# Kernel optimization log

Hardware: AMD Instinct MI355X
Metric: run time of the kernel (lower is better)

The kernel has to match this reference:

```python
import jax, jax.numpy as jnp
import numpy as np

B, T, D, H = 4, 2048, 1024, 8
HD = D // H  # head_dim = 128


def setup_inputs() -> dict:
    key = jax.random.key(0)
    ks = jax.random.split(key, 10)
    s = 1.0 / np.sqrt(D)
    return {
        "x": jax.random.normal(ks[0], (B, T, D), jnp.float32),
        "y": jax.random.normal(ks[1], (B, T, D), jnp.float32),
        "Wq": jax.random.normal(ks[2], (D, D), jnp.float32) * s,
        "bq": jnp.zeros((D,), jnp.float32),
        "Wk": jax.random.normal(ks[3], (D, D), jnp.float32) * s,
        "bk": jnp.zeros((D,), jnp.float32),
        "Wv": jax.random.normal(ks[4], (D, D), jnp.float32) * s,
        "bv": jnp.zeros((D,), jnp.float32),
        "Wo": jax.random.normal(ks[5], (D, D), jnp.float32) * s,
        "bo": jnp.zeros((D,), jnp.float32),
    }


def _heads(t):
    # [B, T, D] -> [B, H, T, HD]
    b, t_, _ = t.shape
    return t.reshape(b, t_, H, HD).transpose(0, 2, 1, 3)


def reference(x, y, Wq, bq, Wk, bk, Wv, bv, Wo, bo):
    Tq, Tk = x.shape[1], y.shape[1]
    q = _heads(x @ Wq.T + bq)  # [B,H,Tq,HD]
    k = _heads(y @ Wk.T + bk)  # [B,H,Tk,HD]
    v = _heads(y @ Wv.T + bv)  # [B,H,Tk,HD]
    scale = 1.0 / np.sqrt(HD)
    logits = jnp.einsum("bhqd,bhkd->bhqk", q, k) * scale
    # causal mask: positions k > q get -inf
    causal = jnp.triu(jnp.full((Tq, Tk), -jnp.inf, jnp.float32), k=1)
    logits = logits + causal
    attn = jax.nn.softmax(logits, axis=-1)  # [B,H,Tq,Tk]
    ctx = jnp.einsum("bhqk,bhkd->bhqd", attn, v)
    ctx = ctx.transpose(0, 2, 1, 3).reshape(x.shape[0], Tq, D)
    out = ctx @ Wo.T + bo
    return out
```

## Files before the change

### kernel.cpp

```cpp
#include <hip/hip_runtime.h>
#include <math.h>

#define TB 4
#define TT 2048
#define TD 1024
#define TH 8
#define THD 128

typedef __attribute__((ext_vector_type(8))) short short8;
typedef __attribute__((ext_vector_type(4))) short short4v;
typedef __attribute__((ext_vector_type(4))) float float4v;
typedef __attribute__((ext_vector_type(16))) float float16v;

__device__ __forceinline__ short f2bf(float f) {
    union { float f; unsigned u; } v; v.f = f;
    unsigned r = v.u + 0x7FFFu + ((v.u >> 16) & 1u);
    return (short)(r >> 16);
}

__device__ __forceinline__ float bf2f(short s) {
    union { unsigned u; float f; } v;
    v.u = ((unsigned)(unsigned short)s) << 16;
    return v.f;
}

__device__ __forceinline__ short8 cvt8(float4v a, float4v b) {
    short8 r;
    r[0] = f2bf(a[0]); r[1] = f2bf(a[1]); r[2] = f2bf(a[2]); r[3] = f2bf(a[3]);
    r[4] = f2bf(b[0]); r[5] = f2bf(b[1]); r[6] = f2bf(b[2]); r[7] = f2bf(b[3]);
    return r;
}

__device__ __forceinline__ void async16(const void* g, void* l) {
    __builtin_amdgcn_global_load_lds(
        (const __attribute__((address_space(1))) unsigned int*)g,
        (__attribute__((address_space(3))) unsigned int*)l, 16, 0, 0);
}

__global__ void cvtall(const float* __restrict__ x, const float* __restrict__ y,
                       const float* __restrict__ wq, const float* __restrict__ wk,
                       const float* __restrict__ wv, const float* __restrict__ wo,
                       short* __restrict__ xyb, short* __restrict__ wb)
{
    const size_t SZ = (size_t)TB * TT * TD;
    const size_t WSZ = (size_t)TD * TD;
    int ty = blockIdx.y;
    const float* s; short* d; size_t n;
    if (ty == 0)      { s = x;  d = xyb;      n = SZ; }
    else if (ty == 1) { s = y;  d = xyb + SZ; n = SZ; }
    else {
        s = (ty == 2) ? wq : (ty == 3) ? wk : (ty == 4) ? wv : wo;
        d = wb + (size_t)(ty - 2) * WSZ; n = WSZ;
    }
    size_t i = ((size_t)blockIdx.x * blockDim.x + threadIdx.x) * 8;
    if (i >= n) return;
    float4v v0 = *(const float4v*)(s + i);
    float4v v1 = *(const float4v*)(s + i + 4);
    *(short8*)(d + i) = cvt8(v0, v1);
}

__global__ __launch_bounds__(256, 2)
void gemm_qkv(const short* __restrict__ xyb, const short* __restrict__ wb,
              const float* __restrict__ bq, const float* __restrict__ bk,
              const float* __restrict__ bv,
              short* __restrict__ qhp, short* __restrict__ khp,
              short* __restrict__ vtp)
{
    __shared__ __attribute__((aligned(16))) short SMEM[16896];
    short* As = SMEM;
    short* Bs = SMEM + 8192;

    const int n0g = blockIdx.x * 128;
    const int mode = n0g >> 10;
    const int n0 = n0g & 1023;
    const int h_ = n0 >> 7;
    const size_t SZ = (size_t)TB * TT * TD;
    const short* A = (mode == 0) ? xyb : (xyb + SZ);
    const short* W = wb + (size_t)mode * TD * TD;
    const float* bias = (mode == 0) ? bq : (mode == 1) ? bk : bv;
    const float scale = (mode == 0)
        ? (0.08838834764831845f * 1.4426950408889634f) : 1.0f;

    const int tid = threadIdx.x;
    const int lane = tid & 63, wv = tid >> 6;
    const int lr = lane & 15, qd = lane >> 4;
    const int sw = lane & 7;
    const int wm = (wv >> 1) * 64, wn = (wv & 1) * 64;
    const int m0 = blockIdx.y * 128;
    const int K = TD;
    const int rsub = lane >> 3;
    const int gj = ((lane & 7) ^ rsub) * 8;

    float4v acc[4][4];
#pragma unroll
    for (int mt = 0; mt < 4; ++mt)
#pragma unroll
        for (int nt = 0; nt < 4; ++nt)
            acc[mt][nt] = float4v{0.f, 0.f, 0.f, 0.f};

    for (int kb = 0; kb < K; kb += 64) {
#pragma unroll
        for (int p = 0; p < 8; ++p) {
            int ch = wv * 8 + p;
            if (ch < 16) {
                int row = ch * 8 + rsub;
                async16(A + (size_t)(m0 + row) * K + kb + gj, As + ch * 512);
            } else {
                int row = (ch - 16) * 8 + rsub;
                async16(W + (size_t)(n0 + row) * K + kb + gj, Bs + (ch - 16) * 512);
            }
        }
        __syncthreads();

#pragma unroll
        for (int ks = 0; ks < 2; ++ks) {
            short8 af[4], bfr[4];
#pragma unroll
            for (int mt = 0; mt < 4; ++mt)
                af[mt] = *(const short8*)&As[(wm + mt * 16 + lr) * 64 +
                                             ((ks * 4 + qd) ^ sw) * 8];
#pragma unroll
            for (int nt = 0; nt < 4; ++nt)
                bfr[nt] = *(const short8*)&Bs[(wn + nt * 16 + lr) * 64 +
                                              ((ks * 4 + qd) ^ sw) * 8];
#pragma unroll
            for (int mt = 0; mt < 4; ++mt)
#pragma unroll
                for (int nt = 0; nt < 4; ++nt)
                    acc[mt][nt] = __builtin_amdgcn_mfma_f32_16x16x32_bf16(
                        af[mt], bfr[nt], acc[mt][nt], 0, 0, 0);
        }
        __syncthreads();
    }

#pragma unroll
    for (int nt = 0; nt < 4; ++nt) {
        int col = wn + nt * 16 + lr;
        float bi = bias[n0 + col];
#pragma unroll
        for (int mt = 0; mt < 4; ++mt)
#pragma unroll
            for (int i = 0; i < 4; ++i) {
                int row = wm + mt * 16 + qd * 4 + i;
                short v = f2bf((acc[mt][nt][i] + bi) * scale);
                if (mode < 2) SMEM[row * 128 + col] = v;
                else          SMEM[col * 132 + row] = v;
            }
    }
    __syncthreads();

    if (mode < 2) {
        short* outp = (mode == 0) ? qhp : khp;
#pragma unroll
        for (int r8 = 0; r8 < 8; ++r8) {
            int row = r8 * 16 + (tid >> 4), c = tid & 15;
            short8 v = *(const short8*)&SMEM[row * 128 + c * 8];
            int tg = m0 + row;
            int b_ = tg >> 11, t_ = tg & (TT - 1);
            *(short8*)&outp[(((size_t)(b_ * TH + h_)) * TT + t_) * THD + c * 8] = v;
        }
    } else {
        int b_ = m0 >> 11, t0 = m0 & (TT - 1);
#pragma unroll
        for (int r8 = 0; r8 < 8; ++r8) {
            int hd = r8 * 16 + (tid >> 4), c = tid & 15;
            short8 v = *(const short8*)&SMEM[hd * 132 + c * 8];
            *(short8*)&vtp[(((size_t)(b_ * TH + h_)) * THD + hd) * TT + t0 + c * 8] = v;
        }
    }
}

__global__ __launch_bounds__(256, 2)
void gemm_out(const short* __restrict__ A, const short* __restrict__ W,
              const float* __restrict__ bias, float* __restrict__ outp)
{
    __shared__ __attribute__((aligned(16))) short As[128 * 64];
    __shared__ __attribute__((aligned(16))) short Bs[128 * 64];

    const int tid = threadIdx.x;
    const int lane = tid & 63, wv = tid >> 6;
    const int lr = lane & 15, qd = lane >> 4;
    const int sw = lane & 7;
    const int wm = (wv >> 1) * 64, wn = (wv & 1) * 64;
    const int m0 = blockIdx.y * 128, n0 = blockIdx.x * 128;
    const int K = TD;
    const int rsub = lane >> 3;
    const int gj = ((lane & 7) ^ rsub) * 8;

    float4v acc[4][4];
#pragma unroll
    for (int mt = 0; mt < 4; ++mt)
#pragma unroll
        for (int nt = 0; nt < 4; ++nt)
            acc[mt][nt] = float4v{0.f, 0.f, 0.f, 0.f};

    for (int kb = 0; kb < K; kb += 64) {
#pragma unroll
        for (int p = 0; p < 8; ++p) {
            int ch = wv * 8 + p;
            if (ch < 16) {
                int row = ch * 8 + rsub;
                async16(A + (size_t)(m0 + row) * K + kb + gj, As + ch * 512);
            } else {
                int row = (ch - 16) * 8 + rsub;
                async16(W + (size_t)(n0 + row) * K + kb + gj, Bs + (ch - 16) * 512);
            }
        }
        __syncthreads();

#pragma unroll
        for (int ks = 0; ks < 2; ++ks) {
            short8 af[4], bfr[4];
#pragma unroll
            for (int mt = 0; mt < 4; ++mt)
                af[mt] = *(const short8*)&As[(wm + mt * 16 + lr) * 64 +
                                             ((ks * 4 + qd) ^ sw) * 8];
#pragma unroll
            for (int nt = 0; nt < 4; ++nt)
                bfr[nt] = *(const short8*)&Bs[(wn + nt * 16 + lr) * 64 +
                                              ((ks * 4 + qd) ^ sw) * 8];
#pragma unroll
            for (int mt = 0; mt < 4; ++mt)
#pragma unroll
                for (int nt = 0; nt < 4; ++nt)
                    acc[mt][nt] = __builtin_amdgcn_mfma_f32_16x16x32_bf16(
                        af[mt], bfr[nt], acc[mt][nt], 0, 0, 0);
        }
        __syncthreads();
    }

#pragma unroll
    for (int nt = 0; nt < 4; ++nt) {
        int col = n0 + wn + nt * 16 + lr;
        float bi = bias[col];
#pragma unroll
        for (int mt = 0; mt < 4; ++mt)
#pragma unroll
            for (int i = 0; i < 4; ++i) {
                int row = m0 + wm + mt * 16 + qd * 4 + i;
                outp[(size_t)row * TD + col] = acc[mt][nt][i] + bi;
            }
    }
}

__global__ __launch_bounds__(256, 2)
void attn_fwd(const short* __restrict__ qh, const short* __restrict__ kh,
              const short* __restrict__ vt, short* __restrict__ po,
              float* __restrict__ pl)
{
    __shared__ __attribute__((aligned(16))) short Ks[2][64 * 128];
    __shared__ __attribute__((aligned(16))) short Vs[2][128 * 64];

    const int tid = threadIdx.x;
    const int lane = tid & 63, wid = tid >> 6;
    const int l31 = lane & 31, h = lane >> 5;
    const int sw7 = l31 & 7;

    const int bi = blockIdx.x;
    const int bh = bi & 31;
    const int j  = bi >> 5;
    const size_t bho = (size_t)bh * TT * THD;

    for (int u = 0; u < 2; ++u) {
        const int qt  = u ? (15 - j) : j;
        const int kv0 = u ? (qt + 1) : 0;
        const int kv1 = u ? (2 * qt + 2) : (j + 1);

        short8 qf[8];
        {
            const short* qp = qh + bho + (size_t)(qt * 128 + wid * 32 + l31) * THD;
#pragma unroll
            for (int ks = 0; ks < 8; ++ks)
                qf[ks] = *(const short8*)(qp + ks * 16 + h * 8);
        }
        float16v o[4];
#pragma unroll
        for (int db = 0; db < 4; ++db)
#pragma unroll
            for (int r = 0; r < 16; ++r) o[db][r] = 0.f;
        float li = 0.f;

        {
            const short* kbase = kh + bho + (size_t)kv0 * 64 * THD;
            const short* vbase = vt + (size_t)bh * THD * TT + (size_t)kv0 * 64;
#pragma unroll
            for (int p = 0; p < 4; ++p) {
                int ch = wid * 4 + p;
                int kr = ch * 4 + (lane >> 4);
                int kg = (lane & 15) ^ (kr & 7);
                async16(kbase + (size_t)kr * THD + kg * 8, &Ks[0][ch * 512]);
                int vr = ch * 8 + (lane >> 3);
                int vg = (lane & 7) ^ (vr & 7);
                async16(vbase + (size_t)vr * TT + vg * 8, &Vs[0][ch * 512]);
            }
        }
        __syncthreads();

        int cur = 0;
        for (int kv = kv0; kv < kv1; ++kv) {
            if (kv + 1 < kv1) {
                const short* kbase = kh + bho + (size_t)(kv + 1) * 64 * THD;
                const short* vbase = vt + (size_t)bh * THD * TT +
                                     (size_t)(kv + 1) * 64;
#pragma unroll
                for (int p = 0; p < 4; ++p) {
                    int ch = wid * 4 + p;
                    int kr = ch * 4 + (lane >> 4);
                    int kg = (lane & 15) ^ (kr & 7);
                    async16(kbase + (size_t)kr * THD + kg * 8,
                            &Ks[cur ^ 1][ch * 512]);
                    int vr = ch * 8 + (lane >> 3);
                    int vg = (lane & 7) ^ (vr & 7);
                    async16(vbase + (size_t)vr * TT + vg * 8,
                            &Vs[cur ^ 1][ch * 512]);
                }
            }

            const short* Kc = Ks[cur];
            const short* Vc = Vs[cur];

            float16v s[2];
#pragma unroll
            for (int kb = 0; kb < 2; ++kb)
#pragma unroll
                for (int r = 0; r < 16; ++r) s[kb][r] = 0.f;
#pragma unroll
            for (int ks = 0; ks < 8; ++ks) {
                int cidx = ((ks * 2 + h) ^ sw7) * 8;
                short8 kf0 = *(const short8*)&Kc[l31 * 128 + cidx];
                short8 kf1 = *(const short8*)&Kc[(32 + l31) * 128 + cidx];
                s[0] = __builtin_amdgcn_mfma_f32_32x32x16_bf16(kf0, qf[ks], s[0], 0, 0, 0);
                s[1] = __builtin_amdgcn_mfma_f32_32x32x16_bf16(kf1, qf[ks], s[1], 0, 0, 0);
            }

            if (kv >= 2 * qt) {
                int q = qt * 128 + wid * 32 + l31;
#pragma unroll
                for (int r = 0; r < 16; ++r) {
                    int key = kv * 64 + (r & 3) + 8 * (r >> 2) + 4 * h;
                    if (key > q) s[0][r] = -1e30f;
                    if (key + 32 > q) s[1][r] = -1e30f;
                }
            }

#pragma unroll
            for (int st = 0; st < 8; ++st) {
                float e0 = exp2f(s[st >> 2][(st & 3) * 4 + 0]);
                float e1 = exp2f(s[st >> 2][(st & 3) * 4 + 1]);
                float e2 = exp2f(s[st >> 2][(st & 3) * 4 + 2]);
                float e3 = exp2f(s[st >> 2][(st & 3) * 4 + 3]);
                li += (e0 + e1) + (e2 + e3);
                short4v ap;
                ap[0] = f2bf(e0); ap[1] = f2bf(e1);
                ap[2] = f2bf(e2); ap[3] = f2bf(e3);
#pragma unroll
                for (int db = 0; db < 4; ++db) {
                    short4v vf = *(const short4v*)&Vc[(db * 32 + l31) * 64 +
                                                      ((st ^ sw7) * 8) + h * 4];
                    o[db] = __builtin_amdgcn_mfma_f32_32x32x8bf16_1k(ap, vf, o[db], 0, 0, 0);
                }
            }
            __syncthreads();
            cur ^= 1;
        }

        li += __shfl_xor(li, 32);
        const int slot = (bh * 16 + qt) * 2 + u;
        if (h == 0) pl[slot * 128 + wid * 32 + l31] = li;
        short* pop = po + (size_t)slot * 16384 + (size_t)(wid * 32) * 128 + l31;
#pragma unroll
        for (int r = 0; r < 16; ++r) {
            int ql = (r & 3) + 8 * (r >> 2) + 4 * h;
#pragma unroll
            for (int db = 0; db < 4; ++db)
                pop[(size_t)ql * 128 + db * 32] = f2bf(o[db][r]);
        }
    }
}

__global__ __launch_bounds__(256)
void combine(const short* __restrict__ po, const float* __restrict__ pl,
             short* __restrict__ ctx)
{
    const unsigned i = blockIdx.x * 256 + threadIdx.x;
    const int hdv = i & 15;
    const int q   = (i >> 4) & 127;
    const int qt  = (i >> 11) & 15;
    const int bh  = i >> 15;
    const int tile = bh * 16 + qt;
    const size_t base = (size_t)tile * 2 * 16384 + (size_t)q * 128 + hdv * 8;
    short8 a = *(const short8*)&po[base];
    short8 b = *(const short8*)&po[base + 16384];
    const float inv = 1.f / (pl[tile * 2 * 128 + q] + pl[(tile * 2 + 1) * 128 + q]);
    short8 r;
#pragma unroll
    for (int k = 0; k < 8; ++k)
        r[k] = f2bf((bf2f(a[k]) + bf2f(b[k])) * inv);
    const int b_ = bh >> 3, h_ = bh & 7, t = qt * 128 + q;
    *(short8*)&ctx[((size_t)(b_ * TT + t)) * TD + h_ * THD + hdv * 8] = r;
}

extern "C" void kernel_launch(void* const* d_in, const int* in_sizes, int n_in,
                              void* d_out, int out_size, void* d_ws, size_t ws_size,
                              hipStream_t stream) {
    (void)in_sizes; (void)n_in; (void)out_size; (void)ws_size;
    const float* x  = (const float*)d_in[0];
    const float* y  = (const float*)d_in[1];
    const float* Wq = (const float*)d_in[2];
    const float* bq = (const float*)d_in[3];
    const float* Wk = (const float*)d_in[4];
    const float* bk = (const float*)d_in[5];
    const float* Wv = (const float*)d_in[6];
    const float* bv = (const float*)d_in[7];
    const float* Wo = (const float*)d_in[8];
    const float* bo = (const float*)d_in[9];
    float* out = (float*)d_out;

    const size_t SZ = (size_t)TB * TT * TD;
    const size_t WSZ = (size_t)TD * TD;
    short* xyb = (short*)d_ws;
    short* wb  = xyb + 2 * SZ;
    short* qh  = wb + 4 * WSZ;
    short* kh  = qh + SZ;
    short* vt  = kh + SZ;
    float* pl  = (float*)(vt + SZ);
    short* po  = xyb;
    short* ctx = qh;

    dim3 blk(256);

    hipLaunchKernelGGL(cvtall, dim3(SZ / 2048, 6), blk, 0, stream,
                       x, y, Wq, Wk, Wv, Wo, xyb, wb);
    hipLaunchKernelGGL(gemm_qkv, dim3(24, 64), blk, 0, stream,
                       xyb, wb, bq, bk, bv, qh, kh, vt);
    hipLaunchKernelGGL(attn_fwd, dim3(512), blk, 0, stream, qh, kh, vt, po, pl);
    hipLaunchKernelGGL(combine, dim3(4096), blk, 0, stream, po, pl, ctx);
    hipLaunchKernelGGL(gemm_out, dim3(8, 64), blk, 0, stream,
                       ctx, wb + 3 * WSZ, bo, out);
}
```

Baseline: 292.9 us.

## Rewrite projection GEMMs as 256x128 double-buffered 8-wave pipelined kernels

Replaces the QKV and output projection GEMMs with a shared 512-thread core that computes 256x128 tiles. It double-buffers LDS with async global-to-LDS loads issued two k-steps ahead, interleaves those loads with MFMA phases, and uses explicit waitcnt, barriers and setprio. Block IDs are remapped so that blocks sharing operands are grouped, improving L2 reuse. This aims to hide memory latency and the barrier stalls of the old single-buffer loop, at the cost of more LDS per block (96KB), which limits occupancy, and of fragile hand-tuned synchronization.

```diff
diff --git a/kernel.cpp b/kernel.cpp
--- a/kernel.cpp
+++ b/kernel.cpp
@@ -59,92 +59,204 @@
     *(short8*)(d + i) = cvt8(v0, v1);
 }
 
-__global__ __launch_bounds__(256, 2)
-void gemm_qkv(const short* __restrict__ xyb, const short* __restrict__ wb,
-              const float* __restrict__ bq, const float* __restrict__ bk,
-              const float* __restrict__ bv,
-              short* __restrict__ qhp, short* __restrict__ khp,
-              short* __restrict__ vtp)
+__device__ __forceinline__ void gemm_core256(const short* __restrict__ A,
+                                             const short* __restrict__ W,
+                                             int m0, int n0, short* SM,
+                                             float4v acc[4][4])
 {
-    __shared__ __attribute__((aligned(16))) short SMEM[16896];
-    short* As = SMEM;
-    short* Bs = SMEM + 8192;
-
-    const int n0g = blockIdx.x * 128;
-    const int mode = n0g >> 10;
-    const int n0 = n0g & 1023;
+    short* As = SM;
+    short* Bs = SM + 32768;
+    const int tid = threadIdx.x;
+    const int lane = tid & 63, wid = tid >> 6;
+    const int lr = lane & 15, qd = lane >> 4, sw = lane & 7;
+    const int wr = wid >> 1, wc = wid & 1;
+    const int rsub = lane >> 3;
+    const int gj = ((lane & 7) ^ rsub) * 8;
+    const int K = TD;
+
+    const short* aSrc[4]; int aDst[4];
+    const short* bSrc[2]; int bDst[2];
+#pragma unroll
+    for (int p = 0; p < 4; ++p) {
+        int ch = wid * 4 + p;
+        aSrc[p] = A + (size_t)(m0 + ch * 8 + rsub) * K + gj;
+        aDst[p] = ch * 512;
+    }
+#pragma unroll
+    for (int p = 0; p < 2; ++p) {
+        int ch = wid * 2 + p;
+        bSrc[p] = W + (size_t)(n0 + ch * 8 + rsub) * K + gj;
+        bDst[p] = ch * 512;
+    }
+
+#pragma unroll
+    for (int mt = 0; mt < 4; ++mt)
+#pragma unroll
+        for (int nt = 0; nt < 4; ++nt)
+            acc[mt][nt] = float4v{0.f, 0.f, 0.f, 0.f};
+
+#pragma unroll
+    for (int t = 0; t < 2; ++t) {
+#pragma unroll
+        for (int p = 0; p < 4; ++p)
+            async16(aSrc[p] + t * 64, As + t * 16384 + aDst[p]);
+#pragma unroll
+        for (int p = 0; p < 2; ++p)
+            async16(bSrc[p] + t * 64, Bs + t * 8192 + bDst[p]);
+    }
+    asm volatile("s_waitcnt vmcnt(6)" ::: "memory");
+    __builtin_amdgcn_sched_barrier(0);
+    __builtin_amdgcn_s_barrier();
+
+#pragma unroll 2
+    for (int it = 0; it < 16; ++it) {
+        const short* Ac = As + (it & 1) * 16384;
+        const short* Bc = Bs + (it & 1) * 8192;
+        short* Asn = As + (it & 1) * 16384;
+        short* Bsn = Bs + (it & 1) * 8192;
+        const int kb2 = (it + 2) * 64;
+        const bool stg = (it < 14);
+
+        short8 af[4][2], bf[4][2];
+
+#pragma unroll
+        for (int mi = 0; mi < 2; ++mi)
+#pragma unroll
+            for (int ks = 0; ks < 2; ++ks)
+                af[mi][ks] = *(const short8*)&Ac[(wr * 64 + mi * 16 + lr) * 64 +
+                                                 (((ks * 4 + qd) ^ sw) * 8)];
+#pragma unroll
+        for (int ni = 0; ni < 2; ++ni)
+#pragma unroll
+            for (int ks = 0; ks < 2; ++ks)
+                bf[ni][ks] = *(const short8*)&Bc[(wc * 64 + ni * 16 + lr) * 64 +
+                                                 (((ks * 4 + qd) ^ sw) * 8)];
+        asm volatile("s_waitcnt lgkmcnt(0)" ::: "memory");
+        __builtin_amdgcn_sched_barrier(0);
+        __builtin_amdgcn_s_setprio(1);
+#pragma unroll
+        for (int mi = 0; mi < 2; ++mi)
+#pragma unroll
+            for (int ni = 0; ni < 2; ++ni)
+#pragma unroll
+                for (int ks = 0; ks < 2; ++ks)
+                    acc[mi][ni] = __builtin_amdgcn_mfma_f32_16x16x32_bf16(
+                        af[mi][ks], bf[ni][ks], acc[mi][ni], 0, 0, 0);
+        __builtin_amdgcn_s_setprio(0);
+        __builtin_amdgcn_sched_barrier(0);
+        __builtin_amdgcn_s_barrier();
+
+#pragma unroll
+        for (int mi = 2; mi < 4; ++mi)
+#pragma unroll
+            for (int ks = 0; ks < 2; ++ks)
+                af[mi][ks] = *(const short8*)&Ac[(wr * 64 + mi * 16 + lr) * 64 +
+                                                 (((ks * 4 + qd) ^ sw) * 8)];
+        asm volatile("s_waitcnt lgkmcnt(0)" ::: "memory");
+        __builtin_amdgcn_sched_barrier(0);
+        __builtin_amdgcn_s_setprio(1);
+#pragma unroll
+        for (int mi = 2; mi < 4; ++mi)
+#pragma unroll
+            for (int ni = 0; ni < 2; ++ni)
+#pragma unroll
+                for (int ks = 0; ks < 2; ++ks)
+                    acc[mi][ni] = __builtin_amdgcn_mfma_f32_16x16x32_bf16(
+                        af[mi][ks], bf[ni][ks], acc[mi][ni], 0, 0, 0);
+        __builtin_amdgcn_s_setprio(0);
+        __builtin_amdgcn_sched_barrier(0);
+        __builtin_amdgcn_s_barrier();
+
+        if (stg) {
+#pragma unroll
+            for (int p = 0; p < 4; ++p)
+                async16(aSrc[p] + kb2, Asn + aDst[p]);
+        }
+#pragma unroll
+        for (int ni = 2; ni < 4; ++ni)
+#pragma unroll
+            for (int ks = 0; ks < 2; ++ks)
+                bf[ni][ks] = *(const short8*)&Bc[(wc * 64 + ni * 16 + lr) * 64 +
+                                                 (((ks * 4 + qd) ^ sw) * 8)];
+        asm volatile("s_waitcnt lgkmcnt(0)" ::: "memory");
+        __builtin_amdgcn_sched_barrier(0);
+        __builtin_amdgcn_s_setprio(1);
+#pragma unroll
+        for (int mi = 2; mi < 4; ++mi)
+#pragma unroll
+            for (int ni = 2; ni < 4; ++ni)
+#pragma unroll
+                for (int ks = 0; ks < 2; ++ks)
+                    acc[mi][ni] = __builtin_amdgcn_mfma_f32_16x16x32_bf16(
+                        af[mi][ks], bf[ni][ks], acc[mi][ni], 0, 0, 0);
+        __builtin_amdgcn_s_setprio(0);
+        __builtin_amdgcn_sched_barrier(0);
+        __builtin_amdgcn_s_barrier();
+
+        if (stg) {
+#pragma unroll
+            for (int p = 0; p < 2; ++p)
+                async16(bSrc[p] + kb2, Bsn + bDst[p]);
+        }
+        __builtin_amdgcn_s_setprio(1);
+#pragma unroll
+        for (int mi = 0; mi < 2; ++mi)
+#pragma unroll
+            for (int ni = 2; ni < 4; ++ni)
+#pragma unroll
+                for (int ks = 0; ks < 2; ++ks)
+                    acc[mi][ni] = __builtin_amdgcn_mfma_f32_16x16x32_bf16(
+                        af[mi][ks], bf[ni][ks], acc[mi][ni], 0, 0, 0);
+        __builtin_amdgcn_s_setprio(0);
+        if (stg) { asm volatile("s_waitcnt vmcnt(6)" ::: "memory"); }
+        else     { asm volatile("s_waitcnt vmcnt(0)" ::: "memory"); }
+        __builtin_amdgcn_sched_barrier(0);
+        __builtin_amdgcn_s_barrier();
+    }
+}
+
+__global__ __launch_bounds__(512, 2)
+void gemm_qkv8(const short* __restrict__ xyb, const short* __restrict__ wb,
+               const float* __restrict__ bq, const float* __restrict__ bk,
+               const float* __restrict__ bv,
+               short* __restrict__ qhp, short* __restrict__ khp,
+               short* __restrict__ vtp)
+{
+    __shared__ __attribute__((aligned(16))) short SM[49152];
+    const size_t SZ = (size_t)TB * TT * TD;
+    const int bid = blockIdx.x;
+    const int lin = (bid & 7) * 96 + (bid >> 3);
+    const int by = lin / 24, bx = lin - by * 24;
+    const int mode = bx >> 3;
+    const int n0 = (bx & 7) * 128;
     const int h_ = n0 >> 7;
-    const size_t SZ = (size_t)TB * TT * TD;
+    const int m0 = by * 256;
     const short* A = (mode == 0) ? xyb : (xyb + SZ);
     const short* W = wb + (size_t)mode * TD * TD;
     const float* bias = (mode == 0) ? bq : (mode == 1) ? bk : bv;
     const float scale = (mode == 0)
         ? (0.08838834764831845f * 1.4426950408889634f) : 1.0f;
 
+    float4v acc[4][4];
+    gemm_core256(A, W, m0, n0, SM, acc);
+
     const int tid = threadIdx.x;
-    const int lane = tid & 63, wv = tid >> 6;
+    const int lane = tid & 63, wid = tid >> 6;
     const int lr = lane & 15, qd = lane >> 4;
-    const int sw = lane & 7;
-    const int wm = (wv >> 1) * 64, wn = (wv & 1) * 64;
-    const int m0 = blockIdx.y * 128;
-    const int K = TD;
-    const int rsub = lane >> 3;
-    const int gj = ((lane & 7) ^ rsub) * 8;
-
-    float4v acc[4][4];
-#pragma unroll
-    for (int mt = 0; mt < 4; ++mt)
-#pragma unroll
-        for (int nt = 0; nt < 4; ++nt)
-            acc[mt][nt] = float4v{0.f, 0.f, 0.f, 0.f};
-
-    for (int kb = 0; kb < K; kb += 64) {
-#pragma unroll
-        for (int p = 0; p < 8; ++p) {
-            int ch = wv * 8 + p;
-            if (ch < 16) {
-                int row = ch * 8 + rsub;
-                async16(A + (size_t)(m0 + row) * K + kb + gj, As + ch * 512);
-            } else {
-                int row = (ch - 16) * 8 + rsub;
-                async16(W + (size_t)(n0 + row) * K + kb + gj, Bs + (ch - 16) * 512);
-            }
-        }
-        __syncthreads();
-
-#pragma unroll
-        for (int ks = 0; ks < 2; ++ks) {
-            short8 af[4], bfr[4];
-#pragma unroll
-            for (int mt = 0; mt < 4; ++mt)
-                af[mt] = *(const short8*)&As[(wm + mt * 16 + lr) * 64 +
-                                             ((ks * 4 + qd) ^ sw) * 8];
-#pragma unroll
-            for (int nt = 0; nt < 4; ++nt)
-                bfr[nt] = *(const short8*)&Bs[(wn + nt * 16 + lr) * 64 +
-                                              ((ks * 4 + qd) ^ sw) * 8];
-#pragma unroll
-            for (int mt = 0; mt < 4; ++mt)
-#pragma unroll
-                for (int nt = 0; nt < 4; ++nt)
-                    acc[mt][nt] = __builtin_amdgcn_mfma_f32_16x16x32_bf16(
-                        af[mt], bfr[nt], acc[mt][nt], 0, 0, 0);
-        }
-        __syncthreads();
-    }
+    const int wr = wid >> 1, wc = wid & 1;
 
 #pragma unroll
     for (int nt = 0; nt < 4; ++nt) {
-        int col = wn + nt * 16 + lr;
+        int col = wc * 64 + nt * 16 + lr;
         float bi = bias[n0 + col];
 #pragma unroll
         for (int mt = 0; mt < 4; ++mt)
 #pragma unroll
             for (int i = 0; i < 4; ++i) {
-                int row = wm + mt * 16 + qd * 4 + i;
+                int row = wr * 64 + mt * 16 + qd * 4 + i;
                 short v = f2bf((acc[mt][nt][i] + bi) * scale);
-                if (mode < 2) SMEM[row * 128 + col] = v;
-                else          SMEM[col * 132 + row] = v;
+                if (mode < 2) SM[row * 128 + col] = v;
+                else          SM[col * 264 + row] = v;
             }
     }
     __syncthreads();
@@ -153,8 +265,8 @@
         short* outp = (mode == 0) ? qhp : khp;
 #pragma unroll
         for (int r8 = 0; r8 < 8; ++r8) {
-            int row = r8 * 16 + (tid >> 4), c = tid & 15;
-            short8 v = *(const short8*)&SMEM[row * 128 + c * 8];
+            int row = r8 * 32 + (tid >> 4), c = tid & 15;
+            short8 v = *(const short8*)&SM[row * 128 + c * 8];
             int tg = m0 + row;
             int b_ = tg >> 11, t_ = tg & (TT - 1);
             *(short8*)&outp[(((size_t)(b_ * TH + h_)) * TT + t_) * THD + c * 8] = v;
@@ -163,81 +275,39 @@
         int b_ = m0 >> 11, t0 = m0 & (TT - 1);
 #pragma unroll
         for (int r8 = 0; r8 < 8; ++r8) {
-            int hd = r8 * 16 + (tid >> 4), c = tid & 15;
-            short8 v = *(const short8*)&SMEM[hd * 132 + c * 8];
+            int hd = r8 * 16 + (tid >> 5), c = tid & 31;
+            short8 v = *(const short8*)&SM[hd * 264 + c * 8];
             *(short8*)&vtp[(((size_t)(b_ * TH + h_)) * THD + hd) * TT + t0 + c * 8] = v;
         }
     }
 }
 
-__global__ __launch_bounds__(256, 2)
-void gemm_out(const short* __restrict__ A, const short* __restrict__ W,
-              const float* __restrict__ bias, float* __restrict__ outp)
+__global__ __launch_bounds__(512, 2)
+void gemm_out8(const short* __restrict__ A, const short* __restrict__ W,
+               const float* __restrict__ bias, float* __restrict__ outp)
 {
-    __shared__ __attribute__((aligned(16))) short As[128 * 64];
-    __shared__ __attribute__((aligned(16))) short Bs[128 * 64];
+    __shared__ __attribute__((aligned(16))) short SM[49152];
+    const int bid = blockIdx.x;
+    const int lin = (bid & 7) * 32 + (bid >> 3);
+    const int by = lin >> 3, bx = lin & 7;
+    const int m0 = by * 256, n0 = bx * 128;
+
+    float4v acc[4][4];
+    gemm_core256(A, W, m0, n0, SM, acc);
 
     const int tid = threadIdx.x;
-    const int lane = tid & 63, wv = tid >> 6;
+    const int lane = tid & 63, wid = tid >> 6;
     const int lr = lane & 15, qd = lane >> 4;
-    const int sw = lane & 7;
-    const int wm = (wv >> 1) * 64, wn = (wv & 1) * 64;
-    const int m0 = blockIdx.y * 128, n0 = blockIdx.x * 128;
-    const int K = TD;
-    const int rsub = lane >> 3;
-    const int gj = ((lane & 7) ^ rsub) * 8;
-
-    float4v acc[4][4];
-#pragma unroll
-    for (int mt = 0; mt < 4; ++mt)
-#pragma unroll
-        for (int nt = 0; nt < 4; ++nt)
-            acc[mt][nt] = float4v{0.f, 0.f, 0.f, 0.f};
-
-    for (int kb = 0; kb < K; kb += 64) {
-#pragma unroll
-        for (int p = 0; p < 8; ++p) {
-            int ch = wv * 8 + p;
-            if (ch < 16) {
-                int row = ch * 8 + rsub;
-                async16(A + (size_t)(m0 + row) * K + kb + gj, As + ch * 512);
-            } else {
-                int row = (ch - 16) * 8 + rsub;
-                async16(W + (size_t)(n0 + row) * K + kb + gj, Bs + (ch - 16) * 512);
-            }
-        }
-        __syncthreads();
-
-#pragma unroll
-        for (int ks = 0; ks < 2; ++ks) {
-            short8 af[4], bfr[4];
-#pragma unroll
-            for (int mt = 0; mt < 4; ++mt)
-                af[mt] = *(const short8*)&As[(wm + mt * 16 + lr) * 64 +
-                                             ((ks * 4 + qd) ^ sw) * 8];
-#pragma unroll
-            for (int nt = 0; nt < 4; ++nt)
-                bfr[nt] = *(const short8*)&Bs[(wn + nt * 16 + lr) * 64 +
-                                              ((ks * 4 + qd) ^ sw) * 8];
-#pragma unroll
-            for (int mt = 0; mt < 4; ++mt)
-#pragma unroll
-                for (int nt = 0; nt < 4; ++nt)
-                    acc[mt][nt] = __builtin_amdgcn_mfma_f32_16x16x32_bf16(
-                        af[mt], bfr[nt], acc[mt][nt], 0, 0, 0);
-        }
-        __syncthreads();
-    }
-
+    const int wr = wid >> 1, wc = wid & 1;
 #pragma unroll
     for (int nt = 0; nt < 4; ++nt) {
-        int col = n0 + wn + nt * 16 + lr;
+        int col = n0 + wc * 64 + nt * 16 + lr;
         float bi = bias[col];
 #pragma unroll
         for (int mt = 0; mt < 4; ++mt)
 #pragma unroll
             for (int i = 0; i < 4; ++i) {
-                int row = m0 + wm + mt * 16 + qd * 4 + i;
+                int row = m0 + wr * 64 + mt * 16 + qd * 4 + i;
                 outp[(size_t)row * TD + col] = acc[mt][nt][i] + bi;
             }
     }
@@ -427,14 +497,12 @@
     short* po  = xyb;
     short* ctx = qh;
 
-    dim3 blk(256);
-
-    hipLaunchKernelGGL(cvtall, dim3(SZ / 2048, 6), blk, 0, stream,
+    hipLaunchKernelGGL(cvtall, dim3(SZ / 2048, 6), dim3(256), 0, stream,
                        x, y, Wq, Wk, Wv, Wo, xyb, wb);
-    hipLaunchKernelGGL(gemm_qkv, dim3(24, 64), blk, 0, stream,
+    hipLaunchKernelGGL(gemm_qkv8, dim3(768), dim3(512), 0, stream,
                        xyb, wb, bq, bk, bv, qh, kh, vt);
-    hipLaunchKernelGGL(attn_fwd, dim3(512), blk, 0, stream, qh, kh, vt, po, pl);
-    hipLaunchKernelGGL(combine, dim3(4096), blk, 0, stream, po, pl, ctx);
-    hipLaunchKernelGGL(gemm_out, dim3(8, 64), blk, 0, stream,
+    hipLaunchKernelGGL(attn_fwd, dim3(512), dim3(256), 0, stream, qh, kh, vt, po, pl);
+    hipLaunchKernelGGL(combine, dim3(4096), dim3(256), 0, stream, po, pl, ctx);
+    hipLaunchKernelGGL(gemm_out8, dim3(256), dim3(512), 0, stream,
                        ctx, wb + 3 * WSZ, bo, out);
 }
```

Result: no change. 290.6 us (-0.8%).
